# Kernel optimization log

Hardware: AMD Instinct MI355X
Metric: run time of the kernel (lower is better)

## Reference

```python
import jax, jax.numpy as jnp
import numpy as np

# Dims: N=64 batch, C=256 channels (C4=64 per branch), V=25 joints, T=128 frames,
# K=3 adjacency kernels, Tk=5 temporal kernel, part=4 (3 active branches).
N, C, V, T = 64, 256, 25, 128
K, TK = 3, 5
C4 = C // 4
BRANCHES = 3  # part - 1
EPS = 1e-5
NEG_SLOPE = 0.2


def setup_inputs() -> dict:
    key = jax.random.key(0)
    ks = jax.random.split(key, 9)
    x = jax.random.normal(ks[0], (N, C, V, T), jnp.float32)
    A = jax.random.uniform(ks[1], (K, V, V), jnp.float32)  # adjacency buffer
    conv_w = jax.random.normal(ks[2], (BRANCHES, C4, TK), jnp.float32) * 0.2
    conv_b = jax.random.normal(ks[3], (BRANCHES, C4), jnp.float32) * 0.05
    gconv_w = jax.random.normal(ks[4], (BRANCHES, V, C4 * K, C4), jnp.float32) / jnp.sqrt(jnp.float32(C4))
    bn_gamma = 1.0 + 0.1 * jax.random.normal(ks[5], (BRANCHES, C4), jnp.float32)
    bn_beta = 0.1 * jax.random.normal(ks[6], (BRANCHES, C4), jnp.float32)
    bn_mean = 0.05 * jax.random.normal(ks[7], (BRANCHES, C4), jnp.float32)
    bn_var = 0.75 + 0.5 * jax.random.uniform(ks[8], (BRANCHES, C4), jnp.float32)
    return {"x": x, "A": A, "conv_w": conv_w, "conv_b": conv_b,
            "gconv_w": gconv_w, "bn_gamma": bn_gamma, "bn_beta": bn_beta,
            "bn_mean": bn_mean, "bn_var": bn_var}


def _depthwise_conv_t(s, w, b):
    # s: [N, C4, V, T]; depthwise conv over T per (channel, node), 'same' padding.
    n, c4, v, t = s.shape
    m = s.transpose(0, 2, 1, 3).reshape(n * v, c4, t)  # merge (N,V) into batch
    pad = w.shape[-1] // 2
    y = jax.lax.conv_general_dilated(
        m, w[:, None, :], window_strides=(1,), padding=[(pad, pad)],
        feature_group_count=c4)
    y = y + b[None, :, None]
    return y.reshape(n, v, c4, t).transpose(0, 2, 1, 3)


def _simple_gc(s, Wv, A):
    # s: [N, C4, V, T]; Wv: [V, C4*K, C4] per-node 1x1 grouped conv weight.
    n, c4, v, t = s.shape
    k = A.shape[0]
    y = jnp.einsum('voc,ncvt->novt', Wv, s)          # [N, C4*K, V, T]
    y = y.reshape(n, c4, k, v, t)                    # split out-chans: (C, K), C outer
    return jnp.einsum('kwv,nckwt->ncvt', A, y)       # adjacency contraction


def reference(x, A, conv_w, conv_b, gconv_w, bn_gamma, bn_beta, bn_mean, bn_var):
    n, c, v, t = x.shape
    c4 = c // 4
    splits = jnp.split(x, 4, axis=1)  # four [N, C4, V, T]
    out_parts = []
    acc = None
    for i in range(BRANCHES):
        acc = splits[i] if acc is None else acc + splits[i]
        s = _depthwise_conv_t(acc, conv_w[i], conv_b[i])
        z = _simple_gc(s, gconv_w[i], A)
        # BatchNorm2d (inference) + LeakyReLU(0.2), fused elementwise
        scale = (bn_gamma[i] / jnp.sqrt(bn_var[i] + EPS))[None, :, None, None]
        z = (z - bn_mean[i][None, :, None, None]) * scale + bn_beta[i][None, :, None, None]
        z = jnp.where(z > 0, z, NEG_SLOPE * z)
        out_parts.append(z)
        acc = z
    out_parts.append(splits[3])  # last part passes through untouched
    return jnp.concatenate(out_parts, axis=1)
```

## Files before the change

kernel.cpp:

```cpp
#include <hip/hip_runtime.h>

#define N_   64
#define C4_  64
#define V_   25
#define T_   128
#define K_   3
#define OC_  192

__global__ __launch_bounds__(256)
void k1_acc_conv(const float* __restrict__ x, const float* __restrict__ out,
                 const float* __restrict__ conv_w, const float* __restrict__ conv_b,
                 float* __restrict__ s, int branch) {
    int bid  = blockIdx.x;
    int e    = bid & 7;
    int slot = bid >> 3;
    int n    = e + 8 * (slot / 200);
    int inner = slot % 200;
    int lane = threadIdx.x & 63;
    int wave = threadIdx.x >> 6;
    int rl   = wave * 2 + (lane >> 5);
    int q    = lane & 31;
    int rowv = inner * 8 + rl;
    int c = rowv / 25, v = rowv % 25;

    const float4* xp = (const float4*)(x + ((size_t)(n * 256 + branch * C4_ + c) * V_ + v) * T_);
    float4 a = xp[q];
    if (branch > 0) {
        const float4* zp = (const float4*)(out + ((size_t)(n * 256 + (branch - 1) * C4_ + c) * V_ + v) * T_);
        float4 b = zp[q];
        a.x += b.x; a.y += b.y; a.z += b.z; a.w += b.w;
    }
    float em2 = __shfl_up(a.z, 1, 32);
    float em1 = __shfl_up(a.w, 1, 32);
    float ep1 = __shfl_down(a.x, 1, 32);
    float ep2 = __shfl_down(a.y, 1, 32);
    if (q == 0)  { em2 = 0.f; em1 = 0.f; }
    if (q == 31) { ep1 = 0.f; ep2 = 0.f; }

    const float* wp = conv_w + (branch * C4_ + c) * 5;
    float w0 = wp[0], w1 = wp[1], w2 = wp[2], w3 = wp[3], w4 = wp[4];
    float b0 = conv_b[branch * C4_ + c];
    float4 o;
    o.x = b0 + w0*em2 + w1*em1 + w2*a.x + w3*a.y + w4*a.z;
    o.y = b0 + w0*em1 + w1*a.x + w2*a.y + w3*a.z + w4*a.w;
    o.z = b0 + w0*a.x + w1*a.y + w2*a.z + w3*a.w + w4*ep1;
    o.w = b0 + w0*a.y + w1*a.z + w2*a.w + w3*ep1 + w4*ep2;
    float4* sp = (float4*)(s + ((size_t)(n * C4_ + c) * V_ + v) * T_);
    sp[q] = o;
}

__global__ __launch_bounds__(256, 4)
void k23(const float* __restrict__ s, const float* __restrict__ gW,
         const float* __restrict__ A,
         const float* __restrict__ bng, const float* __restrict__ bnb,
         const float* __restrict__ bnm, const float* __restrict__ bnv,
         float* __restrict__ out, int branch) {
    __shared__ float lds[8192];
    int bid  = blockIdx.x;
    int e    = bid & 7;
    int slot = bid >> 3;
    int n    = e + 8 * (slot >> 4);
    int cg   = slot & 15;
    int wave = threadIdx.x >> 6;
    int lane = threadIdx.x & 63;
    int c    = __builtin_amdgcn_readfirstlane(cg * 4 + wave);
    int t0   = lane * 2;

    const float* sbase = s + (size_t)n * (C4_ * V_ * T_);

    float2 acc[V_];
    #pragma unroll
    for (int v = 0; v < V_; ++v) { acc[v].x = 0.f; acc[v].y = 0.f; }

    auto stage = [&](int pp, int dbase) {
        int w_ = pp >> 1, h_ = pp & 1;
        const float* g0 = sbase + (size_t)(h_ * 32) * (V_ * T_) + (size_t)w_ * T_;
        #pragma unroll
        for (int j = 0; j < 4; ++j) {
            int idx4 = (wave * 4 + j) * 64 + lane;
            int cl = idx4 >> 5, t4 = idx4 & 31;
            const float* gp = g0 + (size_t)cl * (V_ * T_) + t4 * 4;
            __builtin_amdgcn_global_load_lds(
                (const __attribute__((address_space(1))) void*)gp,
                (__attribute__((address_space(3))) void*)&lds[dbase + (wave * 4 + j) * 256],
                16, 0, 0);
        }
    };

    stage(0, 0);
    __syncthreads();

    float2 y0, y1, y2;
    for (int p = 0; p < 50; ++p) {
        int w_ = p >> 1, h = p & 1;
        int cur = (p & 1) * 4096;
        if (p < 49) stage(p + 1, cur ^ 4096);

        const float* Wb = gW + (((size_t)branch * V_ + w_) * OC_ + c * 3) * C4_ + h * 32;
        const float* bp = lds + cur + t0;
        if (h == 0) { y0.x=y0.y=y1.x=y1.y=y2.x=y2.y=0.f; }
        #pragma unroll 8
        for (int cl = 0; cl < 32; ++cl) {
            float2 sv = *(const float2*)(bp + cl * T_);
            float a0 = Wb[cl], a1 = Wb[C4_ + cl], a2 = Wb[2 * C4_ + cl];
            y0.x += a0 * sv.x; y0.y += a0 * sv.y;
            y1.x += a1 * sv.x; y1.y += a1 * sv.y;
            y2.x += a2 * sv.x; y2.y += a2 * sv.y;
        }
        if (h == 1) {
            const float* A0 = A + (0 * V_ + w_) * V_;
            const float* A1 = A + (1 * V_ + w_) * V_;
            const float* A2 = A + (2 * V_ + w_) * V_;
            #pragma unroll
            for (int v = 0; v < V_; ++v) {
                float a0 = A0[v], a1 = A1[v], a2 = A2[v];
                acc[v].x += a0 * y0.x + a1 * y1.x + a2 * y2.x;
                acc[v].y += a0 * y0.y + a1 * y1.y + a2 * y2.y;
            }
        }
        __syncthreads();
    }

    float g  = bng[branch * C4_ + c];
    float be = bnb[branch * C4_ + c];
    float mu = bnm[branch * C4_ + c];
    float va = bnv[branch * C4_ + c];
    float sc = g * rsqrtf(va + 1e-5f);
    float* op = out + ((size_t)(n * 256 + branch * C4_ + c) * V_) * T_ + t0;
    #pragma unroll
    for (int v = 0; v < V_; ++v) {
        float zx = (acc[v].x - mu) * sc + be;
        float zy = (acc[v].y - mu) * sc + be;
        zx = zx > 0.f ? zx : 0.2f * zx;
        zy = zy > 0.f ? zy : 0.2f * zy;
        float2 o2; o2.x = zx; o2.y = zy;
        *(float2*)(op + (size_t)v * T_) = o2;
    }
}

__global__ __launch_bounds__(256)
void k4_copy(const float* __restrict__ x, float* __restrict__ out) {
    int i = blockIdx.x * blockDim.x + threadIdx.x;
    int n = i / 51200;
    int j = i % 51200;
    const float4* src = (const float4*)(x + (size_t)(n * 256 + 192) * (V_ * T_));
    float4* dst = (float4*)(out + (size_t)(n * 256 + 192) * (V_ * T_));
    dst[j] = src[j];
}

extern "C" void kernel_launch(void* const* d_in, const int* in_sizes, int n_in,
                              void* d_out, int out_size, void* d_ws, size_t ws_size,
                              hipStream_t stream) {
    const float* x      = (const float*)d_in[0];
    const float* A      = (const float*)d_in[1];
    const float* conv_w = (const float*)d_in[2];
    const float* conv_b = (const float*)d_in[3];
    const float* gW     = (const float*)d_in[4];
    const float* bng    = (const float*)d_in[5];
    const float* bnb    = (const float*)d_in[6];
    const float* bnm    = (const float*)d_in[7];
    const float* bnv    = (const float*)d_in[8];
    float* out = (float*)d_out;

    float* s = (float*)d_ws;

    for (int i = 0; i < 3; ++i) {
        hipLaunchKernelGGL(k1_acc_conv, dim3(12800), dim3(256), 0, stream,
                           x, out, conv_w, conv_b, s, i);
        hipLaunchKernelGGL(k23, dim3(N_ * 16), dim3(256), 0, stream,
                           s, gW, A, bng, bnb, bnm, bnv, out, i);
    }
    hipLaunchKernelGGL(k4_copy, dim3(12800), dim3(256), 0, stream, x, out);
}
```

Measured before the change: 707.5 us.

## Rework conv thread mapping, batch weight loads, and stage adjacency in LDS

The depthwise conv kernel now has each thread cover two 4-wide chunks of a row, and it fetches halo values with overlapping vector loads instead of cross-lane shuffles. That halves the grid to 6400 blocks. The graph conv kernel now preloads 16 weights per output row into registers before the FMA loop. It also copies the adjacency matrix into padded LDS so the A values are read as float2 from shared memory rather than from global memory. These changes aim to cut redundant global traffic and scalar load latency, at the cost of more registers and extra LDS.

```diff
diff --git a/kernel.cpp b/kernel.cpp
--- a/kernel.cpp
+++ b/kernel.cpp
@@ -14,39 +14,54 @@
     int bid  = blockIdx.x;
     int e    = bid & 7;
     int slot = bid >> 3;
-    int n    = e + 8 * (slot / 200);
-    int inner = slot % 200;
-    int lane = threadIdx.x & 63;
-    int wave = threadIdx.x >> 6;
-    int rl   = wave * 2 + (lane >> 5);
-    int q    = lane & 31;
-    int rowv = inner * 8 + rl;
-    int c = rowv / 25, v = rowv % 25;
-
-    const float4* xp = (const float4*)(x + ((size_t)(n * 256 + branch * C4_ + c) * V_ + v) * T_);
-    float4 a = xp[q];
+    int n    = e + 8 * (slot / 100);
+    int inner = slot % 100;
+    int tid = threadIdx.x;
+    int j   = tid & 15;
+    int rl  = tid >> 4;
+    int rowv = inner * 16 + rl;
+    int c = rowv / 25, v = rowv - c * 25;
+
+    const float* xrow = x + ((size_t)(n * 256 + branch * C4_ + c) * V_ + v) * T_;
+    int ta = j * 4, tb = 64 + j * 4;
+    float2 zz; zz.x = 0.f; zz.y = 0.f;
+    float4 m0 = *(const float4*)(xrow + ta);
+    float4 m1 = *(const float4*)(xrow + tb);
+    float2 l0 = j        ? *(const float2*)(xrow + ta - 2) : zz;
+    float2 r0 =            *(const float2*)(xrow + ta + 4);
+    float2 l1 =            *(const float2*)(xrow + tb - 2);
+    float2 r1 = (j < 15) ? *(const float2*)(xrow + tb + 4) : zz;
     if (branch > 0) {
-        const float4* zp = (const float4*)(out + ((size_t)(n * 256 + (branch - 1) * C4_ + c) * V_ + v) * T_);
-        float4 b = zp[q];
-        a.x += b.x; a.y += b.y; a.z += b.z; a.w += b.w;
-    }
-    float em2 = __shfl_up(a.z, 1, 32);
-    float em1 = __shfl_up(a.w, 1, 32);
-    float ep1 = __shfl_down(a.x, 1, 32);
-    float ep2 = __shfl_down(a.y, 1, 32);
-    if (q == 0)  { em2 = 0.f; em1 = 0.f; }
-    if (q == 31) { ep1 = 0.f; ep2 = 0.f; }
+        const float* zrow = out + ((size_t)(n * 256 + (branch - 1) * C4_ + c) * V_ + v) * T_;
+        float4 p0 = *(const float4*)(zrow + ta);
+        float4 p1 = *(const float4*)(zrow + tb);
+        float2 q0 = j        ? *(const float2*)(zrow + ta - 2) : zz;
+        float2 s0 =            *(const float2*)(zrow + ta + 4);
+        float2 q1 =            *(const float2*)(zrow + tb - 2);
+        float2 s1 = (j < 15) ? *(const float2*)(zrow + tb + 4) : zz;
+        m0.x += p0.x; m0.y += p0.y; m0.z += p0.z; m0.w += p0.w;
+        m1.x += p1.x; m1.y += p1.y; m1.z += p1.z; m1.w += p1.w;
+        l0.x += q0.x; l0.y += q0.y; r0.x += s0.x; r0.y += s0.y;
+        l1.x += q1.x; l1.y += q1.y; r1.x += s1.x; r1.y += s1.y;
+    }
 
     const float* wp = conv_w + (branch * C4_ + c) * 5;
     float w0 = wp[0], w1 = wp[1], w2 = wp[2], w3 = wp[3], w4 = wp[4];
     float b0 = conv_b[branch * C4_ + c];
-    float4 o;
-    o.x = b0 + w0*em2 + w1*em1 + w2*a.x + w3*a.y + w4*a.z;
-    o.y = b0 + w0*em1 + w1*a.x + w2*a.y + w3*a.z + w4*a.w;
-    o.z = b0 + w0*a.x + w1*a.y + w2*a.z + w3*a.w + w4*ep1;
-    o.w = b0 + w0*a.y + w1*a.z + w2*a.w + w3*ep1 + w4*ep2;
-    float4* sp = (float4*)(s + ((size_t)(n * C4_ + c) * V_ + v) * T_);
-    sp[q] = o;
+
+    float4 oa, ob;
+    oa.x = b0 + w0*l0.x + w1*l0.y + w2*m0.x + w3*m0.y + w4*m0.z;
+    oa.y = b0 + w0*l0.y + w1*m0.x + w2*m0.y + w3*m0.z + w4*m0.w;
+    oa.z = b0 + w0*m0.x + w1*m0.y + w2*m0.z + w3*m0.w + w4*r0.x;
+    oa.w = b0 + w0*m0.y + w1*m0.z + w2*m0.w + w3*r0.x + w4*r0.y;
+    ob.x = b0 + w0*l1.x + w1*l1.y + w2*m1.x + w3*m1.y + w4*m1.z;
+    ob.y = b0 + w0*l1.y + w1*m1.x + w2*m1.y + w3*m1.z + w4*m1.w;
+    ob.z = b0 + w0*m1.x + w1*m1.y + w2*m1.z + w3*m1.w + w4*r1.x;
+    ob.w = b0 + w0*m1.y + w1*m1.z + w2*m1.w + w3*r1.x + w4*r1.y;
+
+    float* srow = s + ((size_t)(n * C4_ + c) * V_ + v) * T_;
+    *(float4*)(srow + ta) = oa;
+    *(float4*)(srow + tb) = ob;
 }
 
 __global__ __launch_bounds__(256, 4)
@@ -56,6 +71,7 @@
          const float* __restrict__ bnm, const float* __restrict__ bnv,
          float* __restrict__ out, int branch) {
     __shared__ float lds[8192];
+    __shared__ float A_lds[1952];
     int bid  = blockIdx.x;
     int e    = bid & 7;
     int slot = bid >> 3;
@@ -66,6 +82,11 @@
     int c    = __builtin_amdgcn_readfirstlane(cg * 4 + wave);
     int t0   = lane * 2;
 
+    for (int i = threadIdx.x; i < 1950; i += 256) {
+        int row = i / 26, col = i - row * 26;
+        A_lds[i] = (col < 25) ? A[row * 25 + col] : 0.f;
+    }
+
     const float* sbase = s + (size_t)n * (C4_ * V_ * T_);
 
     float2 acc[V_];
@@ -76,13 +97,13 @@
         int w_ = pp >> 1, h_ = pp & 1;
         const float* g0 = sbase + (size_t)(h_ * 32) * (V_ * T_) + (size_t)w_ * T_;
         #pragma unroll
-        for (int j = 0; j < 4; ++j) {
-            int idx4 = (wave * 4 + j) * 64 + lane;
+        for (int jj = 0; jj < 4; ++jj) {
+            int idx4 = (wave * 4 + jj) * 64 + lane;
             int cl = idx4 >> 5, t4 = idx4 & 31;
             const float* gp = g0 + (size_t)cl * (V_ * T_) + t4 * 4;
             __builtin_amdgcn_global_load_lds(
                 (const __attribute__((address_space(1))) void*)gp,
-                (__attribute__((address_space(3))) void*)&lds[dbase + (wave * 4 + j) * 256],
+                (__attribute__((address_space(3))) void*)&lds[dbase + (wave * 4 + jj) * 256],
                 16, 0, 0);
         }
     };
@@ -99,24 +120,40 @@
         const float* Wb = gW + (((size_t)branch * V_ + w_) * OC_ + c * 3) * C4_ + h * 32;
         const float* bp = lds + cur + t0;
         if (h == 0) { y0.x=y0.y=y1.x=y1.y=y2.x=y2.y=0.f; }
-        #pragma unroll 8
-        for (int cl = 0; cl < 32; ++cl) {
-            float2 sv = *(const float2*)(bp + cl * T_);
-            float a0 = Wb[cl], a1 = Wb[C4_ + cl], a2 = Wb[2 * C4_ + cl];
-            y0.x += a0 * sv.x; y0.y += a0 * sv.y;
-            y1.x += a1 * sv.x; y1.y += a1 * sv.y;
-            y2.x += a2 * sv.x; y2.y += a2 * sv.y;
+        #pragma unroll
+        for (int hb = 0; hb < 2; ++hb) {
+            float wa[16], wb[16], wc[16];
+            #pragma unroll
+            for (int q = 0; q < 16; ++q) {
+                wa[q] = Wb[hb * 16 + q];
+                wb[q] = Wb[C4_ + hb * 16 + q];
+                wc[q] = Wb[2 * C4_ + hb * 16 + q];
+            }
+            #pragma unroll
+            for (int q = 0; q < 16; ++q) {
+                float2 sv = *(const float2*)(bp + (hb * 16 + q) * T_);
+                y0.x += wa[q] * sv.x; y0.y += wa[q] * sv.y;
+                y1.x += wb[q] * sv.x; y1.y += wb[q] * sv.y;
+                y2.x += wc[q] * sv.x; y2.y += wc[q] * sv.y;
+            }
         }
         if (h == 1) {
-            const float* A0 = A + (0 * V_ + w_) * V_;
-            const float* A1 = A + (1 * V_ + w_) * V_;
-            const float* A2 = A + (2 * V_ + w_) * V_;
+            const float* A0l = A_lds + (0 * V_ + w_) * 26;
+            const float* A1l = A_lds + (1 * V_ + w_) * 26;
+            const float* A2l = A_lds + (2 * V_ + w_) * 26;
             #pragma unroll
-            for (int v = 0; v < V_; ++v) {
-                float a0 = A0[v], a1 = A1[v], a2 = A2[v];
-                acc[v].x += a0 * y0.x + a1 * y1.x + a2 * y2.x;
-                acc[v].y += a0 * y0.y + a1 * y1.y + a2 * y2.y;
+            for (int vq = 0; vq < 12; ++vq) {
+                float2 a0 = *(const float2*)(A0l + 2 * vq);
+                float2 a1 = *(const float2*)(A1l + 2 * vq);
+                float2 a2 = *(const float2*)(A2l + 2 * vq);
+                acc[2*vq].x   += a0.x * y0.x + a1.x * y1.x + a2.x * y2.x;
+                acc[2*vq].y   += a0.x * y0.y + a1.x * y1.y + a2.x * y2.y;
+                acc[2*vq+1].x += a0.y * y0.x + a1.y * y1.x + a2.y * y2.x;
+                acc[2*vq+1].y += a0.y * y0.y + a1.y * y1.y + a2.y * y2.y;
             }
+            float a0t = A0l[24], a1t = A1l[24], a2t = A2l[24];
+            acc[24].x += a0t * y0.x + a1t * y1.x + a2t * y2.x;
+            acc[24].y += a0t * y0.y + a1t * y1.y + a2t * y2.y;
         }
         __syncthreads();
     }
@@ -165,7 +202,7 @@
     float* s = (float*)d_ws;
 
     for (int i = 0; i < 3; ++i) {
-        hipLaunchKernelGGL(k1_acc_conv, dim3(12800), dim3(256), 0, stream,
+        hipLaunchKernelGGL(k1_acc_conv, dim3(6400), dim3(256), 0, stream,
                            x, out, conv_w, conv_b, s, i);
         hipLaunchKernelGGL(k23, dim3(N_ * 16), dim3(256), 0, stream,
                            s, gW, A, bng, bnb, bnm, bnv, out, i);
```

New measurement: 771.6 us. 1.09x slower.
